# Kernel tuning notes

Hardware: AMD Instinct MI355X
Metric: run time of the kernel (lower is better)

The kernel has to match this reference:

```python
import jax, jax.numpy as jnp
import numpy as np

GAMMA = 0.99      # discount_factor
LAM = 0.95        # gae_decay
CLIP = 0.2        # clipping_param
LOG_2PI = float(np.log(2.0 * np.pi))

B, T, A = 512, 2048, 16


def setup_inputs() -> dict:
    key = jax.random.key(0)
    ks = jax.random.split(key, 8)
    rewards = jax.random.normal(ks[0], (B, T), dtype=jnp.float32)
    critic_out = jax.random.normal(ks[1], (B, T + 1), dtype=jnp.float32)
    mu = jax.random.normal(ks[2], (B, T, A), dtype=jnp.float32)
    sigma = jax.random.uniform(ks[3], (B, T, A), dtype=jnp.float32) * 0.5 + 0.5
    old_mu = jax.random.normal(ks[4], (B, T, A), dtype=jnp.float32)
    old_sigma = jax.random.uniform(ks[5], (B, T, A), dtype=jnp.float32) * 0.5 + 0.5
    actions = jax.random.normal(ks[6], (B, T, A), dtype=jnp.float32)
    dones = jax.random.randint(ks[7], (B, T), 0, 2, dtype=jnp.int32)
    return {"rewards": rewards, "critic_out": critic_out, "mu": mu, "sigma": sigma,
            "old_mu": old_mu, "old_sigma": old_sigma, "actions": actions, "dones": dones}


def _normal_log_prob(x, mu, sigma):
    return -jnp.log(sigma) - 0.5 * LOG_2PI - 0.5 * jnp.square((x - mu) / sigma)


def _gae(rewards, dones_f, critic_out):
    # td_residuals: rewards + gamma * V[1:] - V[:-1]   -> [B, T]
    td = rewards + GAMMA * critic_out[:, 1:] - critic_out[:, :-1]
    b, t = rewards.shape
    # Reversed recurrence: adv[t] = td[t] + gamma*lam*(1 - done[t+1]) * adv[t+1],
    # for t = T-2 .. 0; adv[T-1] stays 0 (matches original loop bounds).
    xs = (jnp.flip(td[:, : t - 1], axis=1).T,        # [T-1, B]
          jnp.flip(dones_f[:, 1:], axis=1).T)        # [T-1, B]

    def step(carry, x):
        td_t, d_t = x
        adv = td_t + GAMMA * LAM * (1.0 - d_t) * carry
        return adv, adv

    _, advs = jax.lax.scan(step, jnp.zeros((b,), rewards.dtype), xs)
    advs = jnp.flip(advs, axis=0).T                  # [B, T-1]
    return jnp.concatenate([advs, jnp.zeros((b, 1), rewards.dtype)], axis=1)


def reference(rewards, critic_out, mu, sigma, old_mu, old_sigma, actions, dones):
    dones_f = dones.astype(rewards.dtype)
    advantages = _gae(rewards, dones_f, critic_out)          # [B, T]
    lp = _normal_log_prob(actions, mu, sigma)                # [B, T, A]
    old_lp = _normal_log_prob(actions, old_mu, old_sigma)    # [B, T, A]
    ratio = jnp.exp(lp - old_lp)
    clipped = jnp.minimum(jnp.maximum(ratio, 1.0 + CLIP), 1.0 - CLIP)
    adv = advantages[..., None]                              # broadcast over action dim
    obj = jnp.minimum(adv * ratio, adv * clipped)
    entropy = jnp.log(sigma) + 0.5 + 0.5 * LOG_2PI           # Normal entropy, [B, T, A]
    return jnp.mean(obj) + entropy
```

## Files before the change

### kernel.cpp

```cpp
#include <hip/hip_runtime.h>
#include <math.h>

#define BB 512
#define TT 2048
#define AA 16
#define NTOT (512LL * 2048LL * 16LL)
#define GAMMA 0.99f
#define GLAM  0.9405f
#define ENTC  1.4189385332046727f

#define QPB 4
#define NB1 (BB * QPB)
#define NB3 2048

typedef float f32x4 __attribute__((ext_vector_type(4)));

#define NT_LOAD(dst, off, base) \
    asm volatile("global_load_dwordx4 %0, %1, %2 nt" \
                 : "=v"(dst) : "v"(off), "s"(base))
#define C_LOAD(dst, off, base) \
    asm volatile("global_load_dwordx4 %0, %1, %2" \
                 : "=v"(dst) : "v"(off), "s"(base))
#define VM_WAIT_FENCE(n) do { \
    asm volatile("s_waitcnt vmcnt(" #n ")"); \
    __builtin_amdgcn_sched_barrier(0); } while (0)

__device__ __forceinline__ float obj1(float x, float m, float s,
                                      float om, float os, float ad)
{
    float rs  = __builtin_amdgcn_rcpf(s);
    float ros = __builtin_amdgcn_rcpf(os);
    float z   = (x - m) * rs;
    float zo  = (x - om) * ros;
    float d   = 0.5f * (zo * zo - z * z);
    float ratio = os * rs * __expf(d);
    return fminf(ad * ratio, ad * 0.8f);
}

__device__ __forceinline__ double obj4d(f32x4 m, f32x4 s, f32x4 om, f32x4 os,
                                        f32x4 x, float ad)
{
    float o0 = obj1(x.x, m.x, s.x, om.x, os.x, ad);
    float o1 = obj1(x.y, m.y, s.y, om.y, os.y, ad);
    float o2 = obj1(x.z, m.z, s.z, om.z, os.z, ad);
    float o3 = obj1(x.w, m.w, s.w, om.w, os.w, ad);
    return (double)o0 + (double)o1 + (double)o2 + (double)o3;
}

__global__ __launch_bounds__(512) void gae_obj_kernel(
    const float* __restrict__ rewards, const float* __restrict__ vout,
    const int* __restrict__ dones,
    const float* __restrict__ mu, const float* __restrict__ sigma,
    const float* __restrict__ old_mu, const float* __restrict__ old_sigma,
    const float* __restrict__ actions,
    double* __restrict__ partials)
{
    __shared__ float  adv_s[TT];
    __shared__ float  wA[8], wB[8];
    __shared__ double wsum[8];

    const int b    = blockIdx.x >> 2;
    const int q    = blockIdx.x & 3;
    const int tid  = threadIdx.x;
    const int lane = tid & 63;
    const int wave = tid >> 6;

    {
        const float* rw = rewards + (size_t)b * TT;
        const float* V  = vout    + (size_t)b * (TT + 1);
        const int*   dn = dones   + (size_t)b * TT;

        const int t_lo = TT - 4 - 4 * tid;

        f32x4 r4 = *(const f32x4*)(rw + t_lo);
        int4  d4 = *(const int4*)(dn + t_lo);
        int   dt = (tid == 0) ? 1 : dn[t_lo + 4];
        float vv[5];
        #pragma unroll
        for (int j = 0; j < 5; ++j) vv[j] = V[t_lo + j];

        float rr[4] = {r4.x, r4.y, r4.z, r4.w};
        int   dd[5] = {d4.x, d4.y, d4.z, d4.w, dt};

        float ak[4], bk[4];
        float SA = 1.f, SB = 0.f;
        #pragma unroll
        for (int k = 0; k < 4; ++k) {
            const int j = 3 - k;
            float bu = rr[j] + GAMMA * vv[j + 1] - vv[j];
            float au = GLAM * (1.f - (float)dd[j + 1]);
            if (k == 0 && tid == 0) { au = 0.f; bu = 0.f; }
            ak[k] = au; bk[k] = bu;
            SB = au * SB + bu;
            SA = au * SA;
        }

        #pragma unroll
        for (int off = 1; off < 64; off <<= 1) {
            float pA = __shfl_up(SA, off, 64);
            float pB = __shfl_up(SB, off, 64);
            if (lane >= off) { SB = SA * pB + SB; SA = SA * pA; }
        }

        if (lane == 63) { wA[wave] = SA; wB[wave] = SB; }
        __syncthreads();

        float PA = 1.f, PB = 0.f;
        for (int w = 0; w < wave; ++w) {
            float aw = wA[w], bw = wB[w];
            PB = aw * PB + bw;
            PA = aw * PA;
        }

        float EA = __shfl_up(SA, 1, 64);
        float EB = __shfl_up(SB, 1, 64);
        if (lane == 0) { EA = 1.f; EB = 0.f; }

        float x = EA * PB + EB;
        float outb[4];
        #pragma unroll
        for (int k = 0; k < 4; ++k) {
            x = ak[k] * x + bk[k];
            outb[3 - k] = x;
        }
        *(f32x4*)(adv_s + t_lo) = (f32x4){outb[0], outb[1], outb[2], outb[3]};
    }
    __syncthreads();

    const size_t basef4 = (size_t)b * 8192 + (size_t)q * 2048;
    const f32x4* m4  = (const f32x4*)mu        + basef4;
    const f32x4* s4  = (const f32x4*)sigma     + basef4;
    const f32x4* om4 = (const f32x4*)old_mu    + basef4;
    const f32x4* os4 = (const f32x4*)old_sigma + basef4;
    const f32x4* x4  = (const f32x4*)actions   + basef4;
    const float* advq = adv_s + q * 512;

    const int ai = tid >> 2;
    const float Aa = advq[ai];
    const float Ba = advq[ai + 128];
    const float Ca = advq[ai + 256];
    const float Da = advq[ai + 384];

    const uint32_t o0 = (uint32_t)tid * 16u;
    const uint32_t o1 = o0 + 512u * 16u;
    const uint32_t o2 = o0 + 1024u * 16u;
    const uint32_t o3 = o0 + 1536u * 16u;

    f32x4 Am, As, Aom, Aos, Ax;
    f32x4 Bm, Bs, Bom, Bos, Bx;
    f32x4 Cm, Cs, Com, Cos, Cx;
    f32x4 Dm, Ds, Dom, Dos, Dx;

    NT_LOAD(Am, o0, m4);  C_LOAD(As, o0, s4);  NT_LOAD(Aom, o0, om4);
    NT_LOAD(Aos, o0, os4);  NT_LOAD(Ax, o0, x4);
    NT_LOAD(Bm, o1, m4);  C_LOAD(Bs, o1, s4);  NT_LOAD(Bom, o1, om4);
    NT_LOAD(Bos, o1, os4);  NT_LOAD(Bx, o1, x4);
    NT_LOAD(Cm, o2, m4);  C_LOAD(Cs, o2, s4);  NT_LOAD(Com, o2, om4);
    NT_LOAD(Cos, o2, os4);  NT_LOAD(Cx, o2, x4);
    NT_LOAD(Dm, o3, m4);  C_LOAD(Ds, o3, s4);  NT_LOAD(Dom, o3, om4);
    NT_LOAD(Dos, o3, os4);  NT_LOAD(Dx, o3, x4);

    VM_WAIT_FENCE(15);
    double lsum = obj4d(Am, As, Aom, Aos, Ax, Aa);
    VM_WAIT_FENCE(10);
    lsum += obj4d(Bm, Bs, Bom, Bos, Bx, Ba);
    VM_WAIT_FENCE(5);
    lsum += obj4d(Cm, Cs, Com, Cos, Cx, Ca);
    VM_WAIT_FENCE(0);
    lsum += obj4d(Dm, Ds, Dom, Dos, Dx, Da);

    #pragma unroll
    for (int off = 32; off > 0; off >>= 1)
        lsum += __shfl_down(lsum, off, 64);
    if (lane == 0) wsum[wave] = lsum;
    __syncthreads();
    if (tid == 0) {
        double t = 0.0;
        #pragma unroll
        for (int w = 0; w < 8; ++w) t += wsum[w];
        partials[blockIdx.x] = t;
    }
}

__global__ __launch_bounds__(256) void out_kernel(
    const float* __restrict__ sigma, const double* __restrict__ partials,
    float* __restrict__ out)
{
    const int tid  = threadIdx.x;
    const int lane = tid & 63, wave = tid >> 6;

    const uint32_t Q = (uint32_t)(NTOT / 4 / 8);
    const uint32_t v = (uint32_t)blockIdx.x * 256u + (uint32_t)tid;
    const f32x4* s4 = (const f32x4*)sigma;
    f32x4* o4 = (f32x4*)out;

    f32x4 a0, a1, a2, a3, a4, a5, a6, a7;
    C_LOAD(a0, (v + 0u * Q) * 16u, s4);
    C_LOAD(a1, (v + 1u * Q) * 16u, s4);
    C_LOAD(a2, (v + 2u * Q) * 16u, s4);
    C_LOAD(a3, (v + 3u * Q) * 16u, s4);
    C_LOAD(a4, (v + 4u * Q) * 16u, s4);
    C_LOAD(a5, (v + 5u * Q) * 16u, s4);
    C_LOAD(a6, (v + 6u * Q) * 16u, s4);
    C_LOAD(a7, (v + 7u * Q) * 16u, s4);

    double s = 0.0;
    #pragma unroll
    for (int i = 0; i < 8; ++i) s += partials[tid + 256 * i];
    #pragma unroll
    for (int off = 32; off > 0; off >>= 1)
        s += __shfl_down(s, off, 64);
    __shared__ double wsum[4];
    __shared__ float  mc_s;
    if (lane == 0) wsum[wave] = s;
    __syncthreads();
    if (tid == 0)
        mc_s = (float)((wsum[0] + wsum[1] + wsum[2] + wsum[3]) / (double)NTOT)
               + ENTC;
    __syncthreads();
    const float mc = mc_s;

    VM_WAIT_FENCE(0);

    f32x4 r0, r1, r2, r3, r4, r5, r6, r7;
    r0.x = mc + __logf(a0.x); r0.y = mc + __logf(a0.y);
    r0.z = mc + __logf(a0.z); r0.w = mc + __logf(a0.w);
    r1.x = mc + __logf(a1.x); r1.y = mc + __logf(a1.y);
    r1.z = mc + __logf(a1.z); r1.w = mc + __logf(a1.w);
    r2.x = mc + __logf(a2.x); r2.y = mc + __logf(a2.y);
    r2.z = mc + __logf(a2.z); r2.w = mc + __logf(a2.w);
    r3.x = mc + __logf(a3.x); r3.y = mc + __logf(a3.y);
    r3.z = mc + __logf(a3.z); r3.w = mc + __logf(a3.w);
    r4.x = mc + __logf(a4.x); r4.y = mc + __logf(a4.y);
    r4.z = mc + __logf(a4.z); r4.w = mc + __logf(a4.w);
    r5.x = mc + __logf(a5.x); r5.y = mc + __logf(a5.y);
    r5.z = mc + __logf(a5.z); r5.w = mc + __logf(a5.w);
    r6.x = mc + __logf(a6.x); r6.y = mc + __logf(a6.y);
    r6.z = mc + __logf(a6.z); r6.w = mc + __logf(a6.w);
    r7.x = mc + __logf(a7.x); r7.y = mc + __logf(a7.y);
    r7.z = mc + __logf(a7.z); r7.w = mc + __logf(a7.w);

    __builtin_nontemporal_store(r0, o4 + v + 0u * Q);
    __builtin_nontemporal_store(r1, o4 + v + 1u * Q);
    __builtin_nontemporal_store(r2, o4 + v + 2u * Q);
    __builtin_nontemporal_store(r3, o4 + v + 3u * Q);
    __builtin_nontemporal_store(r4, o4 + v + 4u * Q);
    __builtin_nontemporal_store(r5, o4 + v + 5u * Q);
    __builtin_nontemporal_store(r6, o4 + v + 6u * Q);
    __builtin_nontemporal_store(r7, o4 + v + 7u * Q);
}

extern "C" void kernel_launch(void* const* d_in, const int* in_sizes, int n_in,
                              void* d_out, int out_size, void* d_ws, size_t ws_size,
                              hipStream_t stream) {
    const float* rewards   = (const float*)d_in[0];
    const float* critic    = (const float*)d_in[1];
    const float* mu        = (const float*)d_in[2];
    const float* sigma     = (const float*)d_in[3];
    const float* old_mu    = (const float*)d_in[4];
    const float* old_sigma = (const float*)d_in[5];
    const float* actions   = (const float*)d_in[6];
    const int*   dones     = (const int*)d_in[7];
    float* out = (float*)d_out;

    double* partials = (double*)d_ws;

    gae_obj_kernel<<<NB1, 512, 0, stream>>>(rewards, critic, dones,
                                            mu, sigma, old_mu, old_sigma,
                                            actions, partials);
    out_kernel<<<NB3, 256, 0, stream>>>(sigma, partials, out);
}
```

Baseline: 319.3 us.

## Finalize mean via last-block atomic counter, remap blocks, slim output kernel

The first kernel now does the global partial-sum reduction itself: each block bumps an atomic counter and the last block writes the mean, so the output kernel only reads one double. The output kernel doubles its grid and halves per-thread work. Block indices are remapped, presumably to change how blocks spread across XCDs. The mu loads switch from nontemporal to cached loads. It adds a memset launch and an atomic per block, and a longer tail for the last block's reduction.

```diff
diff --git a/kernel.cpp b/kernel.cpp
--- a/kernel.cpp
+++ b/kernel.cpp
@@ -11,7 +11,7 @@
 
 #define QPB 4
 #define NB1 (BB * QPB)
-#define NB3 2048
+#define NB3 4096
 
 typedef float f32x4 __attribute__((ext_vector_type(4)));
 
@@ -53,14 +53,17 @@
     const float* __restrict__ mu, const float* __restrict__ sigma,
     const float* __restrict__ old_mu, const float* __restrict__ old_sigma,
     const float* __restrict__ actions,
-    double* __restrict__ partials)
+    double* __restrict__ partials, unsigned int* __restrict__ counter,
+    double* __restrict__ meanPtr)
 {
     __shared__ float  adv_s[TT];
     __shared__ float  wA[8], wB[8];
     __shared__ double wsum[8];
-
-    const int b    = blockIdx.x >> 2;
-    const int q    = blockIdx.x & 3;
+    __shared__ int    winner_s;
+
+    const uint32_t wg = ((blockIdx.x & 7u) << 8) + ((uint32_t)blockIdx.x >> 3);
+    const int b    = (int)(wg >> 2);
+    const int q    = (int)(wg & 3u);
     const int tid  = threadIdx.x;
     const int lane = tid & 63;
     const int wave = tid >> 6;
@@ -151,13 +154,13 @@
     f32x4 Cm, Cs, Com, Cos, Cx;
     f32x4 Dm, Ds, Dom, Dos, Dx;
 
-    NT_LOAD(Am, o0, m4);  C_LOAD(As, o0, s4);  NT_LOAD(Aom, o0, om4);
+    C_LOAD(Am, o0, m4);  C_LOAD(As, o0, s4);  NT_LOAD(Aom, o0, om4);
     NT_LOAD(Aos, o0, os4);  NT_LOAD(Ax, o0, x4);
-    NT_LOAD(Bm, o1, m4);  C_LOAD(Bs, o1, s4);  NT_LOAD(Bom, o1, om4);
+    C_LOAD(Bm, o1, m4);  C_LOAD(Bs, o1, s4);  NT_LOAD(Bom, o1, om4);
     NT_LOAD(Bos, o1, os4);  NT_LOAD(Bx, o1, x4);
-    NT_LOAD(Cm, o2, m4);  C_LOAD(Cs, o2, s4);  NT_LOAD(Com, o2, om4);
+    C_LOAD(Cm, o2, m4);  C_LOAD(Cs, o2, s4);  NT_LOAD(Com, o2, om4);
     NT_LOAD(Cos, o2, os4);  NT_LOAD(Cx, o2, x4);
-    NT_LOAD(Dm, o3, m4);  C_LOAD(Ds, o3, s4);  NT_LOAD(Dom, o3, om4);
+    C_LOAD(Dm, o3, m4);  C_LOAD(Ds, o3, s4);  NT_LOAD(Dom, o3, om4);
     NT_LOAD(Dos, o3, os4);  NT_LOAD(Dx, o3, x4);
 
     VM_WAIT_FENCE(15);
@@ -178,76 +181,63 @@
         double t = 0.0;
         #pragma unroll
         for (int w = 0; w < 8; ++w) t += wsum[w];
-        partials[blockIdx.x] = t;
+        partials[wg] = t;
+        unsigned int old = __hip_atomic_fetch_add(counter, 1u,
+                                                  __ATOMIC_ACQ_REL,
+                                                  __HIP_MEMORY_SCOPE_AGENT);
+        winner_s = (old == (unsigned int)(NB1 - 1)) ? 1 : 0;
     }
+    __syncthreads();
+
+    if (winner_s) {
+        double s = 0.0;
+        #pragma unroll
+        for (int i = 0; i < 4; ++i) s += partials[tid + 512 * i];
+        #pragma unroll
+        for (int off = 32; off > 0; off >>= 1)
+            s += __shfl_down(s, off, 64);
+        if (lane == 0) wsum[wave] = s;
+        __syncthreads();
+        if (tid == 0) {
+            double t = 0.0;
+            #pragma unroll
+            for (int w = 0; w < 8; ++w) t += wsum[w];
+            *meanPtr = t / (double)NTOT;
+        }
+    }
 }
 
 __global__ __launch_bounds__(256) void out_kernel(
-    const float* __restrict__ sigma, const double* __restrict__ partials,
+    const float* __restrict__ sigma, const double* __restrict__ meanPtr,
     float* __restrict__ out)
 {
-    const int tid  = threadIdx.x;
-    const int lane = tid & 63, wave = tid >> 6;
-
-    const uint32_t Q = (uint32_t)(NTOT / 4 / 8);
+    const int tid = threadIdx.x;
+    const uint32_t Q = (uint32_t)(NTOT / 4 / 4);
     const uint32_t v = (uint32_t)blockIdx.x * 256u + (uint32_t)tid;
+
     const f32x4* s4 = (const f32x4*)sigma;
     f32x4* o4 = (f32x4*)out;
 
-    f32x4 a0, a1, a2, a3, a4, a5, a6, a7;
-    C_LOAD(a0, (v + 0u * Q) * 16u, s4);
-    C_LOAD(a1, (v + 1u * Q) * 16u, s4);
-    C_LOAD(a2, (v + 2u * Q) * 16u, s4);
-    C_LOAD(a3, (v + 3u * Q) * 16u, s4);
-    C_LOAD(a4, (v + 4u * Q) * 16u, s4);
-    C_LOAD(a5, (v + 5u * Q) * 16u, s4);
-    C_LOAD(a6, (v + 6u * Q) * 16u, s4);
-    C_LOAD(a7, (v + 7u * Q) * 16u, s4);
-
-    double s = 0.0;
-    #pragma unroll
-    for (int i = 0; i < 8; ++i) s += partials[tid + 256 * i];
-    #pragma unroll
-    for (int off = 32; off > 0; off >>= 1)
-        s += __shfl_down(s, off, 64);
-    __shared__ double wsum[4];
-    __shared__ float  mc_s;
-    if (lane == 0) wsum[wave] = s;
-    __syncthreads();
-    if (tid == 0)
-        mc_s = (float)((wsum[0] + wsum[1] + wsum[2] + wsum[3]) / (double)NTOT)
-               + ENTC;
-    __syncthreads();
-    const float mc = mc_s;
-
-    VM_WAIT_FENCE(0);
-
-    f32x4 r0, r1, r2, r3, r4, r5, r6, r7;
-    r0.x = mc + __logf(a0.x); r0.y = mc + __logf(a0.y);
-    r0.z = mc + __logf(a0.z); r0.w = mc + __logf(a0.w);
-    r1.x = mc + __logf(a1.x); r1.y = mc + __logf(a1.y);
-    r1.z = mc + __logf(a1.z); r1.w = mc + __logf(a1.w);
-    r2.x = mc + __logf(a2.x); r2.y = mc + __logf(a2.y);
-    r2.z = mc + __logf(a2.z); r2.w = mc + __logf(a2.w);
-    r3.x = mc + __logf(a3.x); r3.y = mc + __logf(a3.y);
-    r3.z = mc + __logf(a3.z); r3.w = mc + __logf(a3.w);
-    r4.x = mc + __logf(a4.x); r4.y = mc + __logf(a4.y);
-    r4.z = mc + __logf(a4.z); r4.w = mc + __logf(a4.w);
-    r5.x = mc + __logf(a5.x); r5.y = mc + __logf(a5.y);
-    r5.z = mc + __logf(a5.z); r5.w = mc + __logf(a5.w);
-    r6.x = mc + __logf(a6.x); r6.y = mc + __logf(a6.y);
-    r6.z = mc + __logf(a6.z); r6.w = mc + __logf(a6.w);
-    r7.x = mc + __logf(a7.x); r7.y = mc + __logf(a7.y);
-    r7.z = mc + __logf(a7.z); r7.w = mc + __logf(a7.w);
-
-    __builtin_nontemporal_store(r0, o4 + v + 0u * Q);
-    __builtin_nontemporal_store(r1, o4 + v + 1u * Q);
-    __builtin_nontemporal_store(r2, o4 + v + 2u * Q);
-    __builtin_nontemporal_store(r3, o4 + v + 3u * Q);
-    __builtin_nontemporal_store(r4, o4 + v + 4u * Q);
-    __builtin_nontemporal_store(r5, o4 + v + 5u * Q);
-    __builtin_nontemporal_store(r6, o4 + v + 6u * Q);
-    __builtin_nontemporal_store(r7, o4 + v + 7u * Q);
+    f32x4 a = s4[v];
+    f32x4 b = s4[v + Q];
+    f32x4 c = s4[v + 2u * Q];
+    f32x4 d = s4[v + 3u * Q];
+    const float mc = (float)(*meanPtr) + ENTC;
+
+    f32x4 oa, ob, oc, od;
+    oa.x = mc + __logf(a.x);  oa.y = mc + __logf(a.y);
+    oa.z = mc + __logf(a.z);  oa.w = mc + __logf(a.w);
+    ob.x = mc + __logf(b.x);  ob.y = mc + __logf(b.y);
+    ob.z = mc + __logf(b.z);  ob.w = mc + __logf(b.w);
+    oc.x = mc + __logf(c.x);  oc.y = mc + __logf(c.y);
+    oc.z = mc + __logf(c.z);  oc.w = mc + __logf(c.w);
+    od.x = mc + __logf(d.x);  od.y = mc + __logf(d.y);
+    od.z = mc + __logf(d.z);  od.w = mc + __logf(d.w);
+
+    __builtin_nontemporal_store(oa, o4 + v);
+    __builtin_nontemporal_store(ob, o4 + v + Q);
+    __builtin_nontemporal_store(oc, o4 + v + 2u * Q);
+    __builtin_nontemporal_store(od, o4 + v + 3u * Q);
 }
 
 extern "C" void kernel_launch(void* const* d_in, const int* in_sizes, int n_in,
@@ -263,10 +253,14 @@
     const int*   dones     = (const int*)d_in[7];
     float* out = (float*)d_out;
 
-    double* partials = (double*)d_ws;
-
+    char* ws = (char*)d_ws;
+    double*       meanPtr  = (double*)ws;
+    unsigned int* counter  = (unsigned int*)(ws + 64);
+    double*       partials = (double*)(ws + 4096);
+
+    hipMemsetAsync(counter, 0, sizeof(unsigned int), stream);
     gae_obj_kernel<<<NB1, 512, 0, stream>>>(rewards, critic, dones,
                                             mu, sigma, old_mu, old_sigma,
-                                            actions, partials);
-    out_kernel<<<NB3, 256, 0, stream>>>(sigma, partials, out);
-}
+                                            actions, partials, counter, meanPtr);
+    out_kernel<<<NB3, 256, 0, stream>>>(sigma, meanPtr, out);
+}
```

After: 419.3 us. 31.3% more time.

## Accumulate block sums with a global atomic and remap block indices across XCDs

Applied to the files above, without the earlier changes.

Each block of the GAE/objective kernel now adds its partial sum straight into one global double with an atomic, rather than writing a partials array. The output kernel then reads a single scalar instead of running a per-block reduction with two barriers. Block IDs are also permuted so consecutive batch rows land on the same XCD, meant to improve cache locality. In exchange it adds a memset launch and contention on one atomic, and the floating-point sum order becomes nondeterministic.

```diff
diff --git a/kernel.cpp b/kernel.cpp
--- a/kernel.cpp
+++ b/kernel.cpp
@@ -53,14 +53,15 @@
     const float* __restrict__ mu, const float* __restrict__ sigma,
     const float* __restrict__ old_mu, const float* __restrict__ old_sigma,
     const float* __restrict__ actions,
-    double* __restrict__ partials)
+    double* __restrict__ total)
 {
     __shared__ float  adv_s[TT];
     __shared__ float  wA[8], wB[8];
     __shared__ double wsum[8];
 
-    const int b    = blockIdx.x >> 2;
-    const int q    = blockIdx.x & 3;
+    const uint32_t wg = ((blockIdx.x & 7u) << 8) + ((uint32_t)blockIdx.x >> 3);
+    const int b    = (int)(wg >> 2);
+    const int q    = (int)(wg & 3u);
     const int tid  = threadIdx.x;
     const int lane = tid & 63;
     const int wave = tid >> 6;
@@ -178,21 +179,22 @@
         double t = 0.0;
         #pragma unroll
         for (int w = 0; w < 8; ++w) t += wsum[w];
-        partials[blockIdx.x] = t;
+        __hip_atomic_fetch_add(total, t, __ATOMIC_RELAXED,
+                               __HIP_MEMORY_SCOPE_AGENT);
     }
 }
 
 __global__ __launch_bounds__(256) void out_kernel(
-    const float* __restrict__ sigma, const double* __restrict__ partials,
+    const float* __restrict__ sigma, const double* __restrict__ total,
     float* __restrict__ out)
 {
-    const int tid  = threadIdx.x;
-    const int lane = tid & 63, wave = tid >> 6;
-
+    const int tid = threadIdx.x;
     const uint32_t Q = (uint32_t)(NTOT / 4 / 8);
     const uint32_t v = (uint32_t)blockIdx.x * 256u + (uint32_t)tid;
     const f32x4* s4 = (const f32x4*)sigma;
     f32x4* o4 = (f32x4*)out;
+
+    const double tot = *total;
 
     f32x4 a0, a1, a2, a3, a4, a5, a6, a7;
     C_LOAD(a0, (v + 0u * Q) * 16u, s4);
@@ -204,21 +206,7 @@
     C_LOAD(a6, (v + 6u * Q) * 16u, s4);
     C_LOAD(a7, (v + 7u * Q) * 16u, s4);
 
-    double s = 0.0;
-    #pragma unroll
-    for (int i = 0; i < 8; ++i) s += partials[tid + 256 * i];
-    #pragma unroll
-    for (int off = 32; off > 0; off >>= 1)
-        s += __shfl_down(s, off, 64);
-    __shared__ double wsum[4];
-    __shared__ float  mc_s;
-    if (lane == 0) wsum[wave] = s;
-    __syncthreads();
-    if (tid == 0)
-        mc_s = (float)((wsum[0] + wsum[1] + wsum[2] + wsum[3]) / (double)NTOT)
-               + ENTC;
-    __syncthreads();
-    const float mc = mc_s;
+    const float mc = (float)(tot / (double)NTOT) + ENTC;
 
     VM_WAIT_FENCE(0);
 
@@ -263,10 +251,11 @@
     const int*   dones     = (const int*)d_in[7];
     float* out = (float*)d_out;
 
-    double* partials = (double*)d_ws;
-
+    double* total = (double*)d_ws;
+
+    hipMemsetAsync(total, 0, sizeof(double), stream);
     gae_obj_kernel<<<NB1, 512, 0, stream>>>(rewards, critic, dones,
                                             mu, sigma, old_mu, old_sigma,
-                                            actions, partials);
-    out_kernel<<<NB3, 256, 0, stream>>>(sigma, partials, out);
-}
+                                            actions, total);
+    out_kernel<<<NB3, 256, 0, stream>>>(sigma, total, out);
+}
```

After: 331.3 us. +3.8%, slower.
